# Kernel tuning notes

Hardware: AMD Instinct MI355X
Metric: run time of the kernel (lower is better)

## Reference

```python
import jax, jax.numpy as jnp
import numpy as np

B, N, DIM = 2, 4096, 1024
DEPTH, HEADS, DHEAD = 6, 8, 128
BUCKET = 64          # blindspot_size -> causal_linear_attn bucket_size
DFF = 4 * DIM
EPS_LN = 1e-5
EPS_ATTN = 1e-3


def setup_inputs() -> dict:
    key = jax.random.key(0)
    ks = jax.random.split(key, 16)
    s = 0.02
    HD = HEADS * DHEAD
    inp = {
        "x":     jax.random.normal(ks[0], (B, N, DIM), jnp.float32),
        "ln1_g": jnp.ones((DEPTH, DIM), jnp.float32),
        "ln1_b": jnp.zeros((DEPTH, DIM), jnp.float32),
        "Wq":    jax.random.normal(ks[1], (DEPTH, DIM, HD), jnp.float32) * s,
        "Wk":    jax.random.normal(ks[2], (DEPTH, DIM, HD), jnp.float32) * s,
        "Wv":    jax.random.normal(ks[3], (DEPTH, DIM, HD), jnp.float32) * s,
        "Wo":    jax.random.normal(ks[4], (DEPTH, HD, DIM), jnp.float32) * s,
        "bo":    jnp.zeros((DEPTH, DIM), jnp.float32),
        "ln2_g": jnp.ones((DEPTH, DIM), jnp.float32),
        "ln2_b": jnp.zeros((DEPTH, DIM), jnp.float32),
        "W1":    jax.random.normal(ks[5], (DEPTH, DIM, DFF), jnp.float32) * s,
        "b1":    jnp.zeros((DEPTH, DFF), jnp.float32),
        "W2":    jax.random.normal(ks[6], (DEPTH, DFF, DIM), jnp.float32) * s,
        "b2":    jnp.zeros((DEPTH, DIM), jnp.float32),
    }
    return inp


def layernorm(x, g, b):
    m = jnp.mean(x, axis=-1, keepdims=True)
    v = jnp.var(x, axis=-1, keepdims=True)
    return (x - m) * jax.lax.rsqrt(v + EPS_LN) * g + b


def causal_linear_attn(q, k, v, bucket_size=BUCKET, eps=EPS_ATTN):
    # q,k,v: [b, h, n, e]; n divisible by bucket_size. Blindspot bucketed causal linear attn.
    b, h, n, e = q.shape
    q = jax.nn.softmax(q, axis=-1) * (e ** -0.5)
    k = jnp.exp(k)
    u = n // bucket_size
    bq = q.reshape(b, h, u, bucket_size, e)
    bk = k.reshape(b, h, u, bucket_size, e)
    bv = v.reshape(b, h, u, bucket_size, e)
    b_k_cumsum = jnp.cumsum(bk.sum(axis=-2), axis=2)                     # [b,h,u,e]
    context = jnp.cumsum(jnp.einsum('bhund,bhune->bhude', bk, bv), axis=2)  # [b,h,u,e,e]
    if bucket_size > 1:
        # shift by one bucket: each bucket only sees strictly earlier buckets (blindspot)
        context = jnp.pad(context, ((0, 0), (0, 0), (1, 0), (0, 0), (0, 0)))[:, :, :-1]
        b_k_cumsum = jnp.pad(b_k_cumsum, ((0, 0), (0, 0), (1, 0), (0, 0)))[:, :, :-1]
    D_inv = 1.0 / jnp.maximum(jnp.einsum('bhud,bhund->bhun', b_k_cumsum, bq), eps)
    out = jnp.einsum('bhund,bhude,bhun->bhune', bq, context, D_inv)
    return out.reshape(b, h, n, e)


def _forward(x, ln1_g, ln1_b, Wq, Wk, Wv, Wo, bo, ln2_g, ln2_b, W1, b1, W2, b2):
    def split_heads(t):  # [b,n,h*e] -> [b,h,n,e]
        return t.reshape(B, N, HEADS, DHEAD).transpose(0, 2, 1, 3)

    def layer(x, p):
        g1, bb1_, wq, wk, wv, wo, bo_, g2, bb2_, w1, bias1, w2, bias2 = p
        h = layernorm(x, g1, bb1_)
        q, k, v = split_heads(h @ wq), split_heads(h @ wk), split_heads(h @ wv)
        a = causal_linear_attn(q, k, v)
        a = a.transpose(0, 2, 1, 3).reshape(B, N, HEADS * DHEAD)
        x = x + a @ wo + bo_
        h = layernorm(x, g2, bb2_)
        x = x + jax.nn.gelu(h @ w1 + bias1, approximate=False) @ w2 + bias2
        return x, None

    params = (ln1_g, ln1_b, Wq, Wk, Wv, Wo, bo, ln2_g, ln2_b, W1, b1, W2, b2)
    x, _ = jax.lax.scan(layer, x, params)
    return x


def reference(x, ln1_g, ln1_b, Wq, Wk, Wv, Wo, bo, ln2_g, ln2_b, W1, b1, W2, b2):
    return _forward(x, ln1_g, ln1_b, Wq, Wk, Wv, Wo, bo, ln2_g, ln2_b, W1, b1, W2, b2)
```

## Files before the change

kernel.cpp:

```cpp
#include <hip/hip_runtime.h>
#include <hip/hip_bf16.h>
#include <stdint.h>

#define TOK 8192
#define DIM 1024
#define NSEQ 4096
#define NH 8
#define DHD 128
#define NU 64
#define DFF 4096
#define NBH 16
#define QKVN 3072

typedef unsigned short u16;
typedef unsigned int u32;
typedef short bf16x8 __attribute__((ext_vector_type(8)));
typedef float f32x4 __attribute__((ext_vector_type(4)));

__device__ __forceinline__ float bu2f(u16 u) { return __uint_as_float(((u32)u) << 16); }
__device__ __forceinline__ u16 f2bu(float f) {
  union { __hip_bfloat16 b; u16 u; } cv; cv.b = __float2bfloat16(f); return cv.u;
}

typedef __attribute__((address_space(1))) void gvoid_t;
typedef __attribute__((address_space(3))) void lvoid_t;
__device__ __forceinline__ void gload16(void* lds, const void* g) {
#if __has_builtin(__builtin_amdgcn_global_load_lds)
  __builtin_amdgcn_global_load_lds((const gvoid_t*)g, (lvoid_t*)lds, 16, 0, 0);
#else
  const int l = threadIdx.x & 63;
  ((uint4*)lds)[l] = *(const uint4*)g;
#endif
}

__global__ __launch_bounds__(256) void wtrans_kernel(const float* __restrict__ W,
    u16* __restrict__ Wt, int K, int N, int dStride, int rowOff)
{
  __shared__ float T[32][33];
  const int tid = threadIdx.x;
  const size_t soff = (size_t)blockIdx.z * K * N;
  const size_t doff = (size_t)blockIdx.z * dStride;
  const int n0 = blockIdx.x << 5, k0 = blockIdx.y << 5;
  const int r = tid >> 3, c4 = (tid & 7) << 2;
  float4 v = *(const float4*)(W + soff + (size_t)(k0 + r) * N + n0 + c4);
  T[r][c4] = v.x; T[r][c4 + 1] = v.y; T[r][c4 + 2] = v.z; T[r][c4 + 3] = v.w;
  __syncthreads();
  u32 lo = (u32)f2bu(T[c4][r]) | ((u32)f2bu(T[c4 + 1][r]) << 16);
  u32 hi = (u32)f2bu(T[c4 + 2][r]) | ((u32)f2bu(T[c4 + 3][r]) << 16);
  *(uint2*)(Wt + doff + (size_t)(rowOff + n0 + r) * K + k0 + c4) = make_uint2(lo, hi);
}

__global__ __launch_bounds__(256) void ln_kernel(const float* __restrict__ x,
    const float* __restrict__ g, const float* __restrict__ bt, u16* __restrict__ h)
{
  const int row = blockIdx.x, tid = threadIdx.x;
  const int w = tid >> 6, l = tid & 63;
  float4 v = ((const float4*)(x + (size_t)row * DIM))[tid];
  float s = v.x + v.y + v.z + v.w;
  float s2 = v.x * v.x + v.y * v.y + v.z * v.z + v.w * v.w;
#pragma unroll
  for (int off = 32; off; off >>= 1) { s += __shfl_down(s, off); s2 += __shfl_down(s2, off); }
  __shared__ float ps[8];
  __shared__ float mv[2];
  if (l == 0) { ps[w] = s; ps[4 + w] = s2; }
  __syncthreads();
  if (tid == 0) {
    float S = ps[0] + ps[1] + ps[2] + ps[3];
    float S2 = ps[4] + ps[5] + ps[6] + ps[7];
    float mean = S * (1.f / 1024.f);
    float var = S2 * (1.f / 1024.f) - mean * mean;
    mv[0] = mean; mv[1] = rsqrtf(var + 1e-5f);
  }
  __syncthreads();
  const float mean = mv[0], inv = mv[1];
  const int c = tid * 4;
  float o0 = (v.x - mean) * inv * g[c + 0] + bt[c + 0];
  float o1 = (v.y - mean) * inv * g[c + 1] + bt[c + 1];
  float o2 = (v.z - mean) * inv * g[c + 2] + bt[c + 2];
  float o3 = (v.w - mean) * inv * g[c + 3] + bt[c + 3];
  u32 lo = (u32)f2bu(o0) | ((u32)f2bu(o1) << 16);
  u32 hi = (u32)f2bu(o2) | ((u32)f2bu(o3) << 16);
  ((uint2*)(h + (size_t)row * DIM))[tid] = make_uint2(lo, hi);
}

template<int EPI>
__global__ __launch_bounds__(256, 2) void gemm_kernel(
    const u16* __restrict__ A, const u16* __restrict__ Bt, void* Cout,
    const float* __restrict__ bias, const float* res, u16* __restrict__ qs,
    u16* __restrict__ ket, u16* __restrict__ vt, float* __restrict__ Ksum,
    int M, int N, int K)
{
  __shared__ __align__(16) u16 As[2][128 * 32];
  __shared__ __align__(16) u16 Bs[2][128 * 32];
  __shared__ float sm[2][128];
  const int tid = threadIdx.x;
  const int w = tid >> 6, l = tid & 63;
  const int gx = gridDim.x;
  const int nwg = gx * gridDim.y;
  const int orig = blockIdx.y * gx + blockIdx.x;
  const int qq = nwg >> 3, rr = nwg & 7, xcd = orig & 7, lin = orig >> 3;
  const int wg = (xcd < rr ? xcd * (qq + 1) : rr * (qq + 1) + (xcd - rr) * qq) + lin;
  const int brow = (wg / gx) << 7, bcol = (wg % gx) << 7;
  const int wr = (w >> 1) << 6, wc = (w & 1) << 6;
  const int lr = l & 15, lk = (l >> 4) << 3;
  f32x4 acc[4][4] = {};
  const int nk = K >> 5;

#define STAGE_G(buf, kt)                                                        \
  {                                                                             \
    _Pragma("unroll")                                                           \
    for (int j = 0; j < 2; ++j) {                                               \
      int c = j * 256 + tid;                                                    \
      int rrow = c >> 2, k8 = (c & 3) << 3;                                     \
      int ub = (j * 256 + w * 64) * 8;                                          \
      gload16(&As[buf][ub], A + (size_t)(brow + rrow) * K + (kt) * 32 + k8);    \
      gload16(&Bs[buf][ub], Bt + (size_t)(bcol + rrow) * K + (kt) * 32 + k8);   \
    }                                                                           \
  }

  STAGE_G(0, 0);
  __syncthreads();
  for (int kt = 0; kt < nk; ++kt) {
    int buf = kt & 1;
    if (kt + 1 < nk) STAGE_G(buf ^ 1, kt + 1);
    bf16x8 a[4], bb[4];
#pragma unroll
    for (int m = 0; m < 4; ++m) a[m] = *(const bf16x8*)&As[buf][(wr + m * 16 + lr) * 32 + lk];
#pragma unroll
    for (int n = 0; n < 4; ++n) bb[n] = *(const bf16x8*)&Bs[buf][(wc + n * 16 + lr) * 32 + lk];
#pragma unroll
    for (int m = 0; m < 4; ++m)
#pragma unroll
      for (int n = 0; n < 4; ++n)
        acc[m][n] = __builtin_amdgcn_mfma_f32_16x16x32_bf16(a[m], bb[n], acc[m][n], 0, 0, 0);
    __syncthreads();
  }
#undef STAGE_G
  const int l4 = (l >> 4) << 2;

  if (EPI == 3) {
    if (bcol < 1024) {
      const int wcol = w & 1;
      float rmax[4][4], rsum[4][4];
#pragma unroll
      for (int m = 0; m < 4; ++m)
#pragma unroll
        for (int r = 0; r < 4; ++r) {
          float v = fmaxf(fmaxf(acc[m][0][r], acc[m][1][r]), fmaxf(acc[m][2][r], acc[m][3][r]));
#pragma unroll
          for (int msk = 1; msk < 16; msk <<= 1) v = fmaxf(v, __shfl_xor(v, msk));
          rmax[m][r] = v;
        }
      __syncthreads();
#pragma unroll
      for (int m = 0; m < 4; ++m)
#pragma unroll
        for (int r = 0; r < 4; ++r) sm[wcol][wr + m * 16 + l4 + r] = rmax[m][r];
      __syncthreads();
#pragma unroll
      for (int m = 0; m < 4; ++m)
#pragma unroll
        for (int r = 0; r < 4; ++r) rmax[m][r] = fmaxf(rmax[m][r], sm[wcol ^ 1][wr + m * 16 + l4 + r]);
#pragma unroll
      for (int m = 0; m < 4; ++m)
#pragma unroll
        for (int r = 0; r < 4; ++r) {
          float s = 0.f;
#pragma unroll
          for (int n = 0; n < 4; ++n) {
            float e = __expf(acc[m][n][r] - rmax[m][r]);
            acc[m][n][r] = e;
            s += e;
          }
#pragma unroll
          for (int msk = 1; msk < 16; msk <<= 1) s += __shfl_xor(s, msk);
          rsum[m][r] = s;
        }
      __syncthreads();
#pragma unroll
      for (int m = 0; m < 4; ++m)
#pragma unroll
        for (int r = 0; r < 4; ++r) sm[wcol][wr + m * 16 + l4 + r] = rsum[m][r];
      __syncthreads();
#pragma unroll
      for (int m = 0; m < 4; ++m)
#pragma unroll
        for (int r = 0; r < 4; ++r) rsum[m][r] += sm[wcol ^ 1][wr + m * 16 + l4 + r];
#pragma unroll
      for (int m = 0; m < 4; ++m)
#pragma unroll
        for (int n = 0; n < 4; ++n) {
          int col = bcol + wc + n * 16 + lr;
#pragma unroll
          for (int r = 0; r < 4; ++r) {
            int row = brow + wr + m * 16 + l4 + r;
            float v = acc[m][n][r] * (0.08838834764831845f / rsum[m][r]);
            qs[(size_t)row * DIM + col] = f2bu(v);
          }
        }
    } else {
      const int isv = (bcol >= 2048);
      const int h = ((bcol - 1024) >> 7) & 7;
      const int b = brow >> 12;
      const int bh = b * 8 + h;
      const int tok0 = brow & 4095;
      u16* dst = isv ? vt : ket;
      float sums[4] = {0.f, 0.f, 0.f, 0.f};
#pragma unroll
      for (int m = 0; m < 4; ++m) {
#pragma unroll
        for (int n = 0; n < 4; ++n) {
          int e = wc + n * 16 + lr;
          int nt = tok0 + wr + m * 16 + l4;
          ushort4 pk;
          float v0 = acc[m][n][0], v1 = acc[m][n][1], v2 = acc[m][n][2], v3 = acc[m][n][3];
          if (!isv) {
            v0 = __expf(v0); v1 = __expf(v1); v2 = __expf(v2); v3 = __expf(v3);
            sums[n] += v0 + v1 + v2 + v3;
          }
          pk.x = f2bu(v0); pk.y = f2bu(v1); pk.z = f2bu(v2); pk.w = f2bu(v3);
          *(ushort4*)(dst + ((size_t)(bh * 128 + e)) * NSEQ + nt) = pk;
        }
      }
      if (!isv) {
        const int u = (tok0 + wr) >> 6;
#pragma unroll
        for (int n = 0; n < 4; ++n) {
          float s = sums[n];
          s += __shfl_xor(s, 16);
          s += __shfl_xor(s, 32);
          if ((l >> 4) == 0)
            Ksum[(((size_t)bh * 64 + u) << 7) + (wc + n * 16 + lr)] = s;
        }
      }
    }
    return;
  }

#pragma unroll
  for (int m = 0; m < 4; ++m) {
#pragma unroll
    for (int n = 0; n < 4; ++n) {
      int col = bcol + wc + n * 16 + lr;
#pragma unroll
      for (int r = 0; r < 4; ++r) {
        int row = brow + wr + m * 16 + l4 + r;
        size_t idx = (size_t)row * N + col;
        float v0 = acc[m][n][r];
        if (EPI == 1) {
          ((float*)Cout)[idx] = v0 + bias[col] + res[idx];
        } else {
          float t = v0 + bias[col];
          float z = 1.5957691216057308f * (t + 0.044715f * t * t * t);
          float e = __expf(z);
          float th = (e - 1.f) / (e + 1.f);
          ((u16*)Cout)[idx] = f2bu(0.5f * t * (1.f + th));
        }
      }
    }
  }
}

__global__ void kc_kernel(const float* __restrict__ Ksum, float* __restrict__ Kc)
{
  const int bh = blockIdx.x, e = threadIdx.x;
  float run = 0.f;
  for (int u = 0; u < 64; ++u) {
    size_t i = (((size_t)bh * 64 + u) << 7) + e;
    Kc[i] = run;
    run += Ksum[i];
  }
}

__global__ __launch_bounds__(256, 2) void ctx_kernel(
    const u16* __restrict__ vt, const u16* __restrict__ ket, u16* __restrict__ ctxT)
{
  __shared__ __align__(16) u16 Av[128 * 64];
  __shared__ __align__(16) u16 Bk[128 * 64];
  const int tid = threadIdx.x, w = tid >> 6, l = tid & 63;
  const int u = blockIdx.x, bh = blockIdx.y;
  const int lr = l & 15, lk = (l >> 4) << 3;
#pragma unroll
  for (int j = 0; j < 4; ++j) {
    int c = j * 256 + tid;
    int row = c >> 3, i8 = (c & 7) << 3;
    size_t goff = ((size_t)(bh * 128 + row)) * NSEQ + u * 64 + i8;
    int ub = (j * 256 + w * 64) * 8;
    gload16(&Av[ub], vt + goff);
    gload16(&Bk[ub], ket + goff);
  }
  __syncthreads();
  const int wr = (w >> 1) << 6, wc = (w & 1) << 6;
  f32x4 acc[4][4] = {};
#pragma unroll
  for (int ks = 0; ks < 2; ++ks) {
    bf16x8 a[4], bb[4];
#pragma unroll
    for (int m = 0; m < 4; ++m) a[m] = *(const bf16x8*)&Av[(wr + m * 16 + lr) * 64 + ks * 32 + lk];
#pragma unroll
    for (int n = 0; n < 4; ++n) bb[n] = *(const bf16x8*)&Bk[(wc + n * 16 + lr) * 64 + ks * 32 + lk];
#pragma unroll
    for (int m = 0; m < 4; ++m)
#pragma unroll
      for (int n = 0; n < 4; ++n)
        acc[m][n] = __builtin_amdgcn_mfma_f32_16x16x32_bf16(a[m], bb[n], acc[m][n], 0, 0, 0);
  }
  u16* out = ctxT + ((size_t)(bh * 64 + u) << 14);
  const int l4 = (l >> 4) << 2;
#pragma unroll
  for (int m = 0; m < 4; ++m)
#pragma unroll
    for (int n = 0; n < 4; ++n)
#pragma unroll
      for (int r = 0; r < 4; ++r) {
        int e = wr + m * 16 + l4 + r, d = wc + n * 16 + lr;
        out[e * 128 + d] = f2bu(acc[m][n][r]);
      }
}

__global__ void cumsum_kernel(const u16* __restrict__ ctxT, u16* __restrict__ ctxc)
{
  const size_t base = ((size_t)blockIdx.y << 20) + (size_t)blockIdx.x * 256 + threadIdx.x;
  const u16* src = ctxT + base;
  u16* dst = ctxc + base;
  float run = 0.f;
  for (int u = 0; u < 64; ++u) {
    u16 cvv = src[(size_t)u << 14];
    dst[(size_t)u << 14] = f2bu(run);
    run += bu2f(cvv);
  }
}

__global__ __launch_bounds__(256, 2) void attnout_kernel(
    const u16* __restrict__ qs, const u16* __restrict__ ctxc,
    const float* __restrict__ Kc, u16* __restrict__ aout)
{
  __shared__ __align__(16) u16 Aq[64 * 128];
  __shared__ __align__(16) u16 Bc[128 * 128];
  __shared__ float KcS[128];
  __shared__ float Dinv[64];
  const int tid = threadIdx.x, w = tid >> 6, l = tid & 63;
  const int u = blockIdx.x, bh = blockIdx.y;
  const int b = bh >> 3, h = bh & 7;
  const int lr = l & 15, lk = (l >> 4) << 3;
#pragma unroll
  for (int j = 0; j < 4; ++j) {
    int c = j * 256 + tid;
    int n = c >> 4, d8 = (c & 15) << 3;
    gload16(&Aq[(j * 256 + w * 64) * 8],
            qs + ((size_t)(b * NSEQ + u * 64 + n)) * DIM + h * 128 + d8);
  }
  const u16* csrc = ctxc + ((size_t)(bh * 64 + u) << 14);
#pragma unroll
  for (int j = 0; j < 8; ++j) {
    int c = j * 256 + tid;
    gload16(&Bc[(j * 256 + w * 64) * 8], csrc + (size_t)c * 8);
  }
  if (tid < 128) KcS[tid] = Kc[(((size_t)bh * 64 + u) << 7) + tid];
  __syncthreads();
  if (tid < 64) {
    float s = 0.f;
#pragma unroll
    for (int dd = 0; dd < 128; ++dd) {
      int d = (dd + tid * 2) & 127;
      s += bu2f(Aq[tid * 128 + d]) * KcS[d];
    }
    Dinv[tid] = 1.f / fmaxf(s, 1e-3f);
  }
  __syncthreads();
  f32x4 acc[4][2] = {};
#pragma unroll
  for (int ks = 0; ks < 4; ++ks) {
    bf16x8 a[4], bb[2];
#pragma unroll
    for (int m = 0; m < 4; ++m) a[m] = *(const bf16x8*)&Aq[(m * 16 + lr) * 128 + ks * 32 + lk];
#pragma unroll
    for (int n = 0; n < 2; ++n) bb[n] = *(const bf16x8*)&Bc[(w * 32 + n * 16 + lr) * 128 + ks * 32 + lk];
#pragma unroll
    for (int m = 0; m < 4; ++m)
#pragma unroll
      for (int n = 0; n < 2; ++n)
        acc[m][n] = __builtin_amdgcn_mfma_f32_16x16x32_bf16(a[m], bb[n], acc[m][n], 0, 0, 0);
  }
  const int l4 = (l >> 4) << 2;
#pragma unroll
  for (int m = 0; m < 4; ++m)
#pragma unroll
    for (int n = 0; n < 2; ++n)
#pragma unroll
      for (int r = 0; r < 4; ++r) {
        int nrow = m * 16 + l4 + r;
        int e = w * 32 + n * 16 + lr;
        float v = acc[m][n][r] * Dinv[nrow];
        aout[((size_t)(b * NSEQ + u * 64 + nrow)) * DIM + h * 128 + e] = f2bu(v);
      }
}

extern "C" void kernel_launch(void* const* d_in, const int* in_sizes, int n_in,
                              void* d_out, int out_size, void* d_ws, size_t ws_size,
                              hipStream_t stream)
{
  (void)in_sizes; (void)n_in; (void)out_size; (void)ws_size;
  const float* x_in = (const float*)d_in[0];
  const float* ln1g = (const float*)d_in[1];
  const float* ln1b = (const float*)d_in[2];
  const float* Wq   = (const float*)d_in[3];
  const float* Wk   = (const float*)d_in[4];
  const float* Wv   = (const float*)d_in[5];
  const float* Wo   = (const float*)d_in[6];
  const float* bo   = (const float*)d_in[7];
  const float* ln2g = (const float*)d_in[8];
  const float* ln2b = (const float*)d_in[9];
  const float* W1   = (const float*)d_in[10];
  const float* b1   = (const float*)d_in[11];
  const float* W2   = (const float*)d_in[12];
  const float* b2   = (const float*)d_in[13];
  float* x = (float*)d_out;

  char* ws = (char*)d_ws;
  size_t off = 0;
  auto alloc = [&](size_t bytes) -> char* {
    char* p = ws + off;
    off += (bytes + 255) & ~(size_t)255;
    return p;
  };
  const size_t SW = (size_t)6 * 1024 * 1024;
  const size_t BW = (size_t)6 * 4096 * 1024;
  u16* Wqkvt = (u16*)alloc(SW * 3 * 2);
  u16* Wot = (u16*)alloc(SW * 2);
  u16* W1t = (u16*)alloc(BW * 2);
  u16* W2t = (u16*)alloc(BW * 2);
  u16* hbuf = (u16*)alloc((size_t)TOK * DIM * 2);
  u16* qsb  = (u16*)alloc((size_t)TOK * DIM * 2);
  u16* ket  = (u16*)alloc((size_t)TOK * DIM * 2);
  u16* vtb  = (u16*)alloc((size_t)TOK * DIM * 2);
  u16* ab   = (u16*)alloc((size_t)TOK * DIM * 2);
  float* Ksum = (float*)alloc((size_t)NBH * 64 * 128 * 4);
  float* Kc   = (float*)alloc((size_t)NBH * 64 * 128 * 4);
  char* R = alloc((size_t)TOK * DFF * 2);
  u16* ctxT = (u16*)R;
  u16* ctxc = (u16*)(R + ((size_t)NBH * 64 * 128 * 128) * 2);
  u16* mid  = (u16*)R;

  wtrans_kernel<<<dim3(32, 32, 6), 256, 0, stream>>>(Wq, Wqkvt, 1024, 1024, QKVN * 1024, 0);
  wtrans_kernel<<<dim3(32, 32, 6), 256, 0, stream>>>(Wk, Wqkvt, 1024, 1024, QKVN * 1024, 1024);
  wtrans_kernel<<<dim3(32, 32, 6), 256, 0, stream>>>(Wv, Wqkvt, 1024, 1024, QKVN * 1024, 2048);
  wtrans_kernel<<<dim3(32, 32, 6), 256, 0, stream>>>(Wo, Wot, 1024, 1024, 1024 * 1024, 0);
  wtrans_kernel<<<dim3(128, 32, 6), 256, 0, stream>>>(W1, W1t, 1024, 4096, 4096 * 1024, 0);
  wtrans_kernel<<<dim3(32, 128, 6), 256, 0, stream>>>(W2, W2t, 4096, 1024, 4096 * 1024, 0);
  (void)hipMemcpyAsync(x, x_in, (size_t)TOK * DIM * 4, hipMemcpyDeviceToDevice, stream);

  for (int d = 0; d < 6; ++d) {
    ln_kernel<<<TOK, 256, 0, stream>>>(x, ln1g + d * DIM, ln1b + d * DIM, hbuf);
    gemm_kernel<3><<<dim3(24, 64), 256, 0, stream>>>(hbuf, Wqkvt + (size_t)d * QKVN * 1024,
        nullptr, nullptr, nullptr, qsb, ket, vtb, Ksum, TOK, QKVN, DIM);
    kc_kernel<<<NBH, 128, 0, stream>>>(Ksum, Kc);
    ctx_kernel<<<dim3(64, NBH), 256, 0, stream>>>(vtb, ket, ctxT);
    cumsum_kernel<<<dim3(64, NBH), 256, 0, stream>>>(ctxT, ctxc);
    attnout_kernel<<<dim3(64, NBH), 256, 0, stream>>>(qsb, ctxc, Kc, ab);
    gemm_kernel<1><<<dim3(8, 64), 256, 0, stream>>>(ab, Wot + (size_t)d * 1024 * 1024, x,
        bo + d * DIM, x, nullptr, nullptr, nullptr, nullptr, TOK, DIM, DIM);
    ln_kernel<<<TOK, 256, 0, stream>>>(x, ln2g + d * DIM, ln2b + d * DIM, hbuf);
    gemm_kernel<2><<<dim3(32, 64), 256, 0, stream>>>(hbuf, W1t + (size_t)d * DFF * 1024, mid,
        b1 + d * DFF, nullptr, nullptr, nullptr, nullptr, nullptr, TOK, DFF, DIM);
    gemm_kernel<1><<<dim3(8, 64), 256, 0, stream>>>(mid, W2t + (size_t)d * DFF * 1024, x,
        b2 + d * DIM, x, nullptr, nullptr, nullptr, nullptr, TOK, DIM, DFF);
  }
}
```

Before: 2.417 ms.

## Split-K the FFN down-projection and fuse partial combine with next LayerNorm

The W2 GEMM (K=4096) now runs as a two-way split-K launch, raising the grid from 512 to 1024 workgroups, and each half writes fp32 partials to a scratch buffer. A new combine kernel sums the partials, adds bias and residual into x, and computes the next layer's LN1 in the same pass, replacing the standalone ln_kernel. This fills more CUs for the down-projection at the cost of extra fp32 partial traffic (two 32MB writes and reads) and a larger workspace. The path is enabled only when the workspace has room for a separate mid buffer.

```diff
diff --git a/kernel.cpp b/kernel.cpp
--- a/kernel.cpp
+++ b/kernel.cpp
@@ -83,12 +83,56 @@
   ((uint2*)(h + (size_t)row * DIM))[tid] = make_uint2(lo, hi);
 }
 
+template<int DO_LN>
+__global__ __launch_bounds__(256) void combine_ln_kernel(const float* __restrict__ P,
+    const float* __restrict__ bias, float* __restrict__ x,
+    const float* __restrict__ g, const float* __restrict__ bt, u16* __restrict__ h)
+{
+  const int row = blockIdx.x, tid = threadIdx.x;
+  const int w = tid >> 6, l = tid & 63;
+  const int c = tid * 4;
+  float4 p0 = ((const float4*)(P + (size_t)row * DIM))[tid];
+  float4 p1 = ((const float4*)(P + (size_t)TOK * DIM + (size_t)row * DIM))[tid];
+  float4 rx = ((const float4*)(x + (size_t)row * DIM))[tid];
+  float4 v;
+  v.x = p0.x + p1.x + bias[c + 0] + rx.x;
+  v.y = p0.y + p1.y + bias[c + 1] + rx.y;
+  v.z = p0.z + p1.z + bias[c + 2] + rx.z;
+  v.w = p0.w + p1.w + bias[c + 3] + rx.w;
+  ((float4*)(x + (size_t)row * DIM))[tid] = v;
+  if (DO_LN == 0) return;
+  float s = v.x + v.y + v.z + v.w;
+  float s2 = v.x * v.x + v.y * v.y + v.z * v.z + v.w * v.w;
+#pragma unroll
+  for (int off = 32; off; off >>= 1) { s += __shfl_down(s, off); s2 += __shfl_down(s2, off); }
+  __shared__ float ps[8];
+  __shared__ float mv[2];
+  if (l == 0) { ps[w] = s; ps[4 + w] = s2; }
+  __syncthreads();
+  if (tid == 0) {
+    float S = ps[0] + ps[1] + ps[2] + ps[3];
+    float S2 = ps[4] + ps[5] + ps[6] + ps[7];
+    float mean = S * (1.f / 1024.f);
+    float var = S2 * (1.f / 1024.f) - mean * mean;
+    mv[0] = mean; mv[1] = rsqrtf(var + 1e-5f);
+  }
+  __syncthreads();
+  const float mean = mv[0], inv = mv[1];
+  float o0 = (v.x - mean) * inv * g[c + 0] + bt[c + 0];
+  float o1 = (v.y - mean) * inv * g[c + 1] + bt[c + 1];
+  float o2 = (v.z - mean) * inv * g[c + 2] + bt[c + 2];
+  float o3 = (v.w - mean) * inv * g[c + 3] + bt[c + 3];
+  u32 lo = (u32)f2bu(o0) | ((u32)f2bu(o1) << 16);
+  u32 hi = (u32)f2bu(o2) | ((u32)f2bu(o3) << 16);
+  ((uint2*)(h + (size_t)row * DIM))[tid] = make_uint2(lo, hi);
+}
+
 template<int EPI>
 __global__ __launch_bounds__(256, 2) void gemm_kernel(
     const u16* __restrict__ A, const u16* __restrict__ Bt, void* Cout,
     const float* __restrict__ bias, const float* res, u16* __restrict__ qs,
     u16* __restrict__ ket, u16* __restrict__ vt, float* __restrict__ Ksum,
-    int M, int N, int K)
+    int M, int N, int K, int klen)
 {
   __shared__ __align__(16) u16 As[2][128 * 32];
   __shared__ __align__(16) u16 Bs[2][128 * 32];
@@ -103,8 +147,9 @@
   const int brow = (wg / gx) << 7, bcol = (wg % gx) << 7;
   const int wr = (w >> 1) << 6, wc = (w & 1) << 6;
   const int lr = l & 15, lk = (l >> 4) << 3;
+  const int ko = (EPI == 4) ? blockIdx.z * klen : 0;
   f32x4 acc[4][4] = {};
-  const int nk = K >> 5;
+  const int nk = klen >> 5;
 
 #define STAGE_G(buf, kt)                                                        \
   {                                                                             \
@@ -113,8 +158,8 @@
       int c = j * 256 + tid;                                                    \
       int rrow = c >> 2, k8 = (c & 3) << 3;                                     \
       int ub = (j * 256 + w * 64) * 8;                                          \
-      gload16(&As[buf][ub], A + (size_t)(brow + rrow) * K + (kt) * 32 + k8);    \
-      gload16(&Bs[buf][ub], Bt + (size_t)(bcol + rrow) * K + (kt) * 32 + k8);   \
+      gload16(&As[buf][ub], A + (size_t)(brow + rrow) * K + ko + (kt) * 32 + k8);  \
+      gload16(&Bs[buf][ub], Bt + (size_t)(bcol + rrow) * K + ko + (kt) * 32 + k8); \
     }                                                                           \
   }
 
@@ -249,6 +294,8 @@
         float v0 = acc[m][n][r];
         if (EPI == 1) {
           ((float*)Cout)[idx] = v0 + bias[col] + res[idx];
+        } else if (EPI == 4) {
+          ((float*)Cout)[(size_t)blockIdx.z * M * N + idx] = v0;
         } else {
           float t = v0 + bias[col];
           float z = 1.5957691216057308f * (t + 0.044715f * t * t * t);
@@ -400,7 +447,7 @@
                               void* d_out, int out_size, void* d_ws, size_t ws_size,
                               hipStream_t stream)
 {
-  (void)in_sizes; (void)n_in; (void)out_size; (void)ws_size;
+  (void)in_sizes; (void)n_in; (void)out_size;
   const float* x_in = (const float*)d_in[0];
   const float* ln1g = (const float*)d_in[1];
   const float* ln1b = (const float*)d_in[2];
@@ -440,7 +487,10 @@
   char* R = alloc((size_t)TOK * DFF * 2);
   u16* ctxT = (u16*)R;
   u16* ctxc = (u16*)(R + ((size_t)NBH * 64 * 128 * 128) * 2);
-  u16* mid  = (u16*)R;
+  char* midbuf = alloc((size_t)TOK * DFF * 2);
+  const bool splitk = (ws_size >= off);
+  u16* mid = splitk ? (u16*)midbuf : (u16*)R;
+  float* P = (float*)R;
 
   wtrans_kernel<<<dim3(32, 32, 6), 256, 0, stream>>>(Wq, Wqkvt, 1024, 1024, QKVN * 1024, 0);
   wtrans_kernel<<<dim3(32, 32, 6), 256, 0, stream>>>(Wk, Wqkvt, 1024, 1024, QKVN * 1024, 1024);
@@ -451,19 +501,34 @@
   (void)hipMemcpyAsync(x, x_in, (size_t)TOK * DIM * 4, hipMemcpyDeviceToDevice, stream);
 
   for (int d = 0; d < 6; ++d) {
-    ln_kernel<<<TOK, 256, 0, stream>>>(x, ln1g + d * DIM, ln1b + d * DIM, hbuf);
+    if (d == 0 || !splitk) {
+      if (d > 0)
+        ln_kernel<<<TOK, 256, 0, stream>>>(x, ln1g + d * DIM, ln1b + d * DIM, hbuf);
+      else
+        ln_kernel<<<TOK, 256, 0, stream>>>(x, ln1g, ln1b, hbuf);
+    } else {
+      combine_ln_kernel<1><<<TOK, 256, 0, stream>>>(P, b2 + (d - 1) * DIM, x,
+          ln1g + d * DIM, ln1b + d * DIM, hbuf);
+    }
     gemm_kernel<3><<<dim3(24, 64), 256, 0, stream>>>(hbuf, Wqkvt + (size_t)d * QKVN * 1024,
-        nullptr, nullptr, nullptr, qsb, ket, vtb, Ksum, TOK, QKVN, DIM);
+        nullptr, nullptr, nullptr, qsb, ket, vtb, Ksum, TOK, QKVN, DIM, DIM);
     kc_kernel<<<NBH, 128, 0, stream>>>(Ksum, Kc);
     ctx_kernel<<<dim3(64, NBH), 256, 0, stream>>>(vtb, ket, ctxT);
     cumsum_kernel<<<dim3(64, NBH), 256, 0, stream>>>(ctxT, ctxc);
     attnout_kernel<<<dim3(64, NBH), 256, 0, stream>>>(qsb, ctxc, Kc, ab);
     gemm_kernel<1><<<dim3(8, 64), 256, 0, stream>>>(ab, Wot + (size_t)d * 1024 * 1024, x,
-        bo + d * DIM, x, nullptr, nullptr, nullptr, nullptr, TOK, DIM, DIM);
+        bo + d * DIM, x, nullptr, nullptr, nullptr, nullptr, TOK, DIM, DIM, DIM);
     ln_kernel<<<TOK, 256, 0, stream>>>(x, ln2g + d * DIM, ln2b + d * DIM, hbuf);
     gemm_kernel<2><<<dim3(32, 64), 256, 0, stream>>>(hbuf, W1t + (size_t)d * DFF * 1024, mid,
-        b1 + d * DFF, nullptr, nullptr, nullptr, nullptr, nullptr, TOK, DFF, DIM);
-    gemm_kernel<1><<<dim3(8, 64), 256, 0, stream>>>(mid, W2t + (size_t)d * DFF * 1024, x,
-        b2 + d * DIM, x, nullptr, nullptr, nullptr, nullptr, TOK, DIM, DFF);
-  }
-}
+        b1 + d * DFF, nullptr, nullptr, nullptr, nullptr, nullptr, TOK, DFF, DIM, DIM);
+    if (splitk) {
+      gemm_kernel<4><<<dim3(8, 64, 2), 256, 0, stream>>>(mid, W2t + (size_t)d * DFF * 1024, P,
+          nullptr, nullptr, nullptr, nullptr, nullptr, nullptr, TOK, DIM, DFF, DFF / 2);
+    } else {
+      gemm_kernel<1><<<dim3(8, 64), 256, 0, stream>>>(mid, W2t + (size_t)d * DFF * 1024, x,
+          b2 + d * DIM, x, nullptr, nullptr, nullptr, nullptr, TOK, DIM, DFF, DFF);
+    }
+  }
+  if (splitk)
+    combine_ln_kernel<0><<<TOK, 256, 0, stream>>>(P, b2 + 5 * DIM, x, nullptr, nullptr, nullptr);
+}
```

Result: faster. 2.340 ms (-3.2%).
